# Kernel optimization log

Measured on AMD Instinct MI355X. Metric: run time of the kernel, lower is better.

Reference implementation:

```python
import jax, jax.numpy as jnp
import numpy as np

NUM_EXPERTS = 8
TOP_K = 2
N_EMBD = 1024
BLOCKING = 128
D_FFN = ((4 * N_EMBD // TOP_K) + BLOCKING - 1) // BLOCKING * BLOCKING  # 2048


def setup_inputs() -> dict:
    key = jax.random.key(0)
    k_x, k_r, k_w1, k_w2 = jax.random.split(key, 4)
    B, S = 4, 2048
    x = jax.random.normal(k_x, (B, S, N_EMBD), dtype=jnp.float32)
    # nn.Linear weight layout: [out_features, in_features]
    router_w = jax.random.normal(k_r, (NUM_EXPERTS, N_EMBD), dtype=jnp.float32) * 0.02
    # trunc_normal(std=0.02, a=-0.06, b=0.06) approximated by clipped normal
    w1 = jnp.clip(jax.random.normal(k_w1, (N_EMBD, NUM_EXPERTS * D_FFN), dtype=jnp.float32) * 0.02, -0.06, 0.06)
    w2 = jnp.clip(jax.random.normal(k_w2, (NUM_EXPERTS * D_FFN, N_EMBD), dtype=jnp.float32) * 0.02, -0.06, 0.06)
    return {"x": x, "router_w": router_w, "w1": w1, "w2": w2}


def reference(x, router_w, w1, w2):
    B, S, D = x.shape
    T = B * S
    x_flat = x.reshape(T, D)

    # Router
    router_logits = x_flat @ router_w.T                       # [T, E]
    router_probs = jax.nn.softmax(router_logits.astype(jnp.float32), axis=-1)
    expert_weights, selected_experts = jax.lax.top_k(router_probs, TOP_K)  # [T, K]
    expert_weights = expert_weights / expert_weights.sum(axis=-1, keepdims=True)
    expert_weights = expert_weights.astype(x.dtype)

    # Combine weights c[t, e] = sum_k weight[t, k] * [sel[t, k] == e]
    combine = jnp.zeros((T, NUM_EXPERTS), dtype=x.dtype)
    combine = combine.at[jnp.arange(T)[:, None], selected_experts].add(expert_weights)

    # Expert FFNs (math equivalent of block-sparse sdd/gelu/dsd + scatter-combine)
    w1r = w1.reshape(D, NUM_EXPERTS, D_FFN)
    w2r = w2.reshape(NUM_EXPERTS, D_FFN, D)
    out_flat = jnp.zeros((T, D), dtype=x.dtype)
    for e in range(NUM_EXPERTS):
        h = jax.nn.gelu(x_flat @ w1r[:, e, :], approximate=False)  # [T, d_ffn]
        out_flat = out_flat + combine[:, e:e + 1] * (h @ w2r[e])
    output = out_flat.reshape(B, S, D)

    # Aux losses
    router_z_loss = jnp.mean(jax.nn.logsumexp(router_logits, axis=-1) ** 2)
    p_i = router_probs.mean(axis=0)                           # [E]
    f_i = jnp.zeros((NUM_EXPERTS,), dtype=x.dtype).at[selected_experts.reshape(-1)].add(
        jnp.float32(1.0) / (T * TOP_K))
    load_balance_loss = NUM_EXPERTS * jnp.dot(f_i, p_i.astype(x.dtype))

    return output, router_z_loss, load_balance_loss, f_i
```

## Files before the change

### kernel.cpp

```cpp
#include <hip/hip_runtime.h>
#include <hip/hip_bf16.h>
#include <math.h>

#define T_TOK   8192
#define D_MODEL 1024
#define DFFN    2048
#define N_EXP   8
#define NASSIGN (T_TOK*2)

#define BM 128
#define BN 128
#define BK 32
#define TILE_MAX 144

#define WS_ZSUM     0
#define WS_PSUM     4
#define WS_COUNTS   64
#define WS_CURSOR   96
#define WS_OFFS     128
#define WS_NTILES   160
#define WS_TMAP     256
#define WS_SEL      4096
#define WS_WGT      69632
#define WS_AIDX     135168
#define WS_AW       200704
#define WS_XB       266240
#define WS_W1T      (WS_XB + 16777216)
#define WS_W2T      (WS_W1T + 33554432)
#define WS_H        (WS_W2T + 33554432)

typedef __attribute__((ext_vector_type(8))) short bf16x8;
typedef __attribute__((ext_vector_type(4))) float f32x4;
typedef __attribute__((ext_vector_type(4))) unsigned int u32x4;

static __device__ __forceinline__ unsigned short f2bf(float f) {
    unsigned int u = __builtin_bit_cast(unsigned int, f);
    u += 0x7fffu + ((u >> 16) & 1u);
    return (unsigned short)(u >> 16);
}

static __device__ __forceinline__ void gll16(const unsigned short* g, unsigned short* l) {
    __builtin_amdgcn_global_load_lds(
        (const __attribute__((address_space(1))) unsigned int*)g,
        (__attribute__((address_space(3))) unsigned int*)l, 16, 0, 0);
}

__global__ __launch_bounds__(256) void cvt_x_kernel(const float* __restrict__ in,
                                                    unsigned short* __restrict__ out)
{
    int i = (blockIdx.x * 256 + threadIdx.x) * 8;
    float4 a = *(const float4*)(in + i);
    float4 b = *(const float4*)(in + i + 4);
    unsigned short t[8];
    t[0]=f2bf(a.x); t[1]=f2bf(a.y); t[2]=f2bf(a.z); t[3]=f2bf(a.w);
    t[4]=f2bf(b.x); t[5]=f2bf(b.y); t[6]=f2bf(b.z); t[7]=f2bf(b.w);
    *(u32x4*)(out + i) = *(u32x4*)t;
}

__global__ __launch_bounds__(256) void transpose_cvt_kernel(
    const float* __restrict__ in, unsigned short* __restrict__ out, int K, int N)
{
    int e = blockIdx.z;
    const float* inp = in + (size_t)e * K * N;
    unsigned short* outp = out + (size_t)e * K * N;
    __shared__ unsigned short tile[64][68];
    int k0 = blockIdx.y * 64, n0 = blockIdx.x * 64;
    int tid = threadIdx.x;
    int r = tid >> 4, c4 = (tid & 15) * 4;
    #pragma unroll
    for (int p = 0; p < 4; ++p) {
        int k = r + p * 16;
        float4 v = *(const float4*)(inp + (size_t)(k0 + k) * N + n0 + c4);
        tile[k][c4+0] = f2bf(v.x);
        tile[k][c4+1] = f2bf(v.y);
        tile[k][c4+2] = f2bf(v.z);
        tile[k][c4+3] = f2bf(v.w);
    }
    __syncthreads();
    int n = tid >> 2, kc = (tid & 3) * 16;
    unsigned short t[16];
    #pragma unroll
    for (int j = 0; j < 16; ++j) t[j] = tile[kc + j][n];
    unsigned short* o = outp + (size_t)(n0 + n) * K + k0 + kc;
    *(u32x4*)o       = *(u32x4*)t;
    *(u32x4*)(o + 8) = *(u32x4*)(t + 8);
}

__global__ __launch_bounds__(256) void router_kernel(
    const float* __restrict__ x, const float* __restrict__ rw,
    float* zsum, float* psum, int* counts, int* sel, float* wgt)
{
    __shared__ float xs[32*129];
    __shared__ float rs[8*129];
    __shared__ float lg[32*9];
    __shared__ float blk_p[8];
    __shared__ int   blk_c[8];
    __shared__ float blk_z;
    int tid = threadIdx.x;
    if (tid < 8) { blk_p[tid] = 0.f; blk_c[tid] = 0; }
    if (tid == 8) blk_z = 0.f;
    int tb = blockIdx.x * 32;
    int tt = tid >> 3, e = tid & 7;
    float acc = 0.f;
    for (int c = 0; c < 8; ++c) {
        int c0 = c * 128;
        #pragma unroll
        for (int p = 0; p < 16; ++p) {
            int flat = p * 256 + tid;
            int r = flat >> 7, col = flat & 127;
            xs[r*129 + col] = x[(size_t)(tb + r)*D_MODEL + c0 + col];
        }
        #pragma unroll
        for (int p = 0; p < 4; ++p) {
            int flat = p * 256 + tid;
            int er = flat >> 7, col = flat & 127;
            rs[er*129 + col] = rw[(size_t)er*D_MODEL + c0 + col];
        }
        __syncthreads();
        #pragma unroll 8
        for (int i = 0; i < 128; ++i)
            acc += xs[tt*129 + i] * rs[e*129 + i];
        __syncthreads();
    }
    lg[tt*9 + e] = acc;
    __syncthreads();
    if (tid < 32) {
        int t = tb + tid;
        float l[8], p[8];
        float mx = -1e30f;
        #pragma unroll
        for (int j = 0; j < 8; ++j) { l[j] = lg[tid*9 + j]; mx = fmaxf(mx, l[j]); }
        float se = 0.f;
        #pragma unroll
        for (int j = 0; j < 8; ++j) { p[j] = expf(l[j] - mx); se += p[j]; }
        float inv = 1.f / se;
        #pragma unroll
        for (int j = 0; j < 8; ++j) p[j] *= inv;
        float lse = mx + logf(se);
        atomicAdd(&blk_z, lse*lse);
        #pragma unroll
        for (int j = 0; j < 8; ++j) atomicAdd(&blk_p[j], p[j]);
        int i0 = 0; float b0 = p[0];
        #pragma unroll
        for (int j = 1; j < 8; ++j) if (p[j] > b0) { b0 = p[j]; i0 = j; }
        int i1 = -1; float b1 = -1.f;
        #pragma unroll
        for (int j = 0; j < 8; ++j) if (j != i0 && p[j] > b1) { b1 = p[j]; i1 = j; }
        float s = b0 + b1;
        sel[t*2+0] = i0; sel[t*2+1] = i1;
        wgt[t*2+0] = b0 / s; wgt[t*2+1] = b1 / s;
        atomicAdd(&blk_c[i0], 1); atomicAdd(&blk_c[i1], 1);
    }
    __syncthreads();
    if (tid < 8) {
        atomicAdd(&counts[tid], blk_c[tid]);
        unsafeAtomicAdd(&psum[tid], blk_p[tid]);
    }
    if (tid == 8) unsafeAtomicAdd(zsum, blk_z);
}

__global__ void finalize_kernel(const int* counts, const float* psum, const float* zsum,
                                int* offs, int* ntiles, int* tmap, float* out_tail)
{
    if (threadIdx.x != 0) return;
    int off = 0, nt = 0;
    float lb = 0.f;
    for (int e = 0; e < N_EXP; ++e) {
        int c = counts[e];
        offs[e] = off;
        for (int m0 = 0; m0 < c; m0 += BM) {
            tmap[nt*4+0] = e;
            tmap[nt*4+1] = off + m0;
            tmap[nt*4+2] = min(BM, c - m0);
            tmap[nt*4+3] = 0;
            nt++;
        }
        float fi = (float)c / (float)NASSIGN;
        out_tail[2 + e] = fi;
        lb += fi * (psum[e] / (float)T_TOK);
        off += c;
    }
    *ntiles = nt;
    out_tail[0] = zsum[0] / (float)T_TOK;
    out_tail[1] = (float)N_EXP * lb;
}

__global__ __launch_bounds__(256) void scatter_kernel(
    const int* __restrict__ sel, const float* __restrict__ wgt,
    const int* __restrict__ offs, int* cursor, int* aidx, float* aw)
{
    int t = blockIdx.x * 256 + threadIdx.x;
    if (t >= T_TOK) return;
    #pragma unroll
    for (int k = 0; k < 2; ++k) {
        int e = sel[t*2 + k];
        int pos = atomicAdd(&cursor[e], 1);
        int r = offs[e] + pos;
        aidx[r] = t;
        aw[r] = wgt[t*2 + k];
    }
}

__global__ __launch_bounds__(256) void gemm1_kernel(
    const unsigned short* __restrict__ xb, const unsigned short* __restrict__ w1t,
    const int* __restrict__ aidx, const int* __restrict__ tmap,
    const int* __restrict__ ntiles, unsigned short* __restrict__ H)
{
    int tile = blockIdx.y;
    if (tile >= *ntiles) return;
    int e     = tmap[tile*4+0];
    int gr    = tmap[tile*4+1];
    int valid = tmap[tile*4+2];
    int n0 = blockIdx.x * BN;
    __shared__ unsigned short As[BM*BK];
    __shared__ unsigned short Bs[BN*BK];
    int tid = threadIdx.x;
    int lane = tid & 63, wave = tid >> 6;
    int wm = (wave & 1) * 64, wn = (wave >> 1) * 64;
    int q = lane >> 4, r16 = lane & 15;
    f32x4 acc[4][4];
    #pragma unroll
    for (int i = 0; i < 4; ++i)
        #pragma unroll
        for (int j = 0; j < 4; ++j) acc[i][j] = (f32x4){0.f, 0.f, 0.f, 0.f};

    int c0 = tid, c1 = 256 + tid;
    int m0c = c0 >> 2, k0c = (c0 & 3) * 8;
    int m1c = c1 >> 2, k1c = (c1 & 3) * 8;
    int tok0 = aidx[gr + min(m0c, valid - 1)];
    int tok1 = aidx[gr + min(m1c, valid - 1)];
    const unsigned short* ga0 = xb + (size_t)tok0 * D_MODEL + k0c;
    const unsigned short* ga1 = xb + (size_t)tok1 * D_MODEL + k1c;
    const unsigned short* gb0 = w1t + ((size_t)(e * DFFN + n0 + m0c)) * D_MODEL + k0c;
    const unsigned short* gb1 = w1t + ((size_t)(e * DFFN + n0 + m1c)) * D_MODEL + k1c;
    unsigned short* lA0 = As + c0 * 8;
    unsigned short* lA1 = As + c1 * 8;
    unsigned short* lB0 = Bs + c0 * 8;
    unsigned short* lB1 = Bs + c1 * 8;

    for (int kt = 0; kt < D_MODEL / BK; ++kt) {
        int kofs = kt * BK;
        gll16(ga0 + kofs, lA0);
        gll16(ga1 + kofs, lA1);
        gll16(gb0 + kofs, lB0);
        gll16(gb1 + kofs, lB1);
        __syncthreads();
        bf16x8 af[4], bfr[4];
        #pragma unroll
        for (int im = 0; im < 4; ++im)
            af[im] = *(const bf16x8*)&As[(wm + im*16 + r16)*BK + q*8];
        #pragma unroll
        for (int in = 0; in < 4; ++in)
            bfr[in] = *(const bf16x8*)&Bs[(wn + in*16 + r16)*BK + q*8];
        #pragma unroll
        for (int im = 0; im < 4; ++im)
            #pragma unroll
            for (int in = 0; in < 4; ++in)
                acc[im][in] = __builtin_amdgcn_mfma_f32_16x16x32_bf16(af[im], bfr[in], acc[im][in], 0, 0, 0);
        __syncthreads();
    }
    #pragma unroll
    for (int im = 0; im < 4; ++im) {
        #pragma unroll
        for (int reg = 0; reg < 4; ++reg) {
            int m = wm + im*16 + q*4 + reg;
            if (m < valid) {
                size_t rowbase = (size_t)(gr + m) * DFFN + n0 + wn;
                #pragma unroll
                for (int in = 0; in < 4; ++in) {
                    float v = acc[im][in][reg];
                    float g = 0.5f * v * (1.0f + erff(v * 0.70710678118654752f));
                    H[rowbase + in*16 + r16] = f2bf(g);
                }
            }
        }
    }
}

__global__ __launch_bounds__(256) void gemm2_kernel(
    const unsigned short* __restrict__ H, const unsigned short* __restrict__ w2t,
    const int* __restrict__ aidx, const float* __restrict__ aw,
    const int* __restrict__ tmap, const int* __restrict__ ntiles,
    float* __restrict__ out)
{
    int tile = blockIdx.y;
    if (tile >= *ntiles) return;
    int e     = tmap[tile*4+0];
    int gr    = tmap[tile*4+1];
    int valid = tmap[tile*4+2];
    int n0 = blockIdx.x * BN;
    __shared__ unsigned short As[BM*BK];
    __shared__ unsigned short Bs[BN*BK];
    int tid = threadIdx.x;
    int lane = tid & 63, wave = tid >> 6;
    int wm = (wave & 1) * 64, wn = (wave >> 1) * 64;
    int q = lane >> 4, r16 = lane & 15;
    f32x4 acc[4][4];
    #pragma unroll
    for (int i = 0; i < 4; ++i)
        #pragma unroll
        for (int j = 0; j < 4; ++j) acc[i][j] = (f32x4){0.f, 0.f, 0.f, 0.f};

    int c0 = tid, c1 = 256 + tid;
    int m0c = c0 >> 2, k0c = (c0 & 3) * 8;
    int m1c = c1 >> 2, k1c = (c1 & 3) * 8;
    const unsigned short* ga0 = H + (size_t)(gr + min(m0c, valid - 1)) * DFFN + k0c;
    const unsigned short* ga1 = H + (size_t)(gr + min(m1c, valid - 1)) * DFFN + k1c;
    const unsigned short* gb0 = w2t + (size_t)e * (DFFN * D_MODEL) + (size_t)(n0 + m0c) * DFFN + k0c;
    const unsigned short* gb1 = w2t + (size_t)e * (DFFN * D_MODEL) + (size_t)(n0 + m1c) * DFFN + k1c;
    unsigned short* lA0 = As + c0 * 8;
    unsigned short* lA1 = As + c1 * 8;
    unsigned short* lB0 = Bs + c0 * 8;
    unsigned short* lB1 = Bs + c1 * 8;

    for (int kt = 0; kt < DFFN / BK; ++kt) {
        int kofs = kt * BK;
        gll16(ga0 + kofs, lA0);
        gll16(ga1 + kofs, lA1);
        gll16(gb0 + kofs, lB0);
        gll16(gb1 + kofs, lB1);
        __syncthreads();
        bf16x8 af[4], bfr[4];
        #pragma unroll
        for (int im = 0; im < 4; ++im)
            af[im] = *(const bf16x8*)&As[(wm + im*16 + r16)*BK + q*8];
        #pragma unroll
        for (int in = 0; in < 4; ++in)
            bfr[in] = *(const bf16x8*)&Bs[(wn + in*16 + r16)*BK + q*8];
        #pragma unroll
        for (int im = 0; im < 4; ++im)
            #pragma unroll
            for (int in = 0; in < 4; ++in)
                acc[im][in] = __builtin_amdgcn_mfma_f32_16x16x32_bf16(af[im], bfr[in], acc[im][in], 0, 0, 0);
        __syncthreads();
    }
    #pragma unroll
    for (int im = 0; im < 4; ++im) {
        #pragma unroll
        for (int reg = 0; reg < 4; ++reg) {
            int m = wm + im*16 + q*4 + reg;
            if (m < valid) {
                int t = aidx[gr + m];
                float w = aw[gr + m];
                float* orow = out + (size_t)t*D_MODEL + n0 + wn;
                #pragma unroll
                for (int in = 0; in < 4; ++in)
                    unsafeAtomicAdd(&orow[in*16 + r16], w * acc[im][in][reg]);
            }
        }
    }
}

extern "C" void kernel_launch(void* const* d_in, const int* in_sizes, int n_in,
                              void* d_out, int out_size, void* d_ws, size_t ws_size,
                              hipStream_t stream)
{
    const float* x  = (const float*)d_in[0];
    const float* rw = (const float*)d_in[1];
    const float* w1 = (const float*)d_in[2];
    const float* w2 = (const float*)d_in[3];
    float* out = (float*)d_out;
    char* ws = (char*)d_ws;
    float* zsum   = (float*)(ws + WS_ZSUM);
    float* psum   = (float*)(ws + WS_PSUM);
    int*   counts = (int*)(ws + WS_COUNTS);
    int*   cursor = (int*)(ws + WS_CURSOR);
    int*   offs   = (int*)(ws + WS_OFFS);
    int*   ntiles = (int*)(ws + WS_NTILES);
    int*   tmap   = (int*)(ws + WS_TMAP);
    int*   sel    = (int*)(ws + WS_SEL);
    float* wgt    = (float*)(ws + WS_WGT);
    int*   aidx   = (int*)(ws + WS_AIDX);
    float* aw     = (float*)(ws + WS_AW);
    unsigned short* xb  = (unsigned short*)(ws + WS_XB);
    unsigned short* w1t = (unsigned short*)(ws + WS_W1T);
    unsigned short* w2t = (unsigned short*)(ws + WS_W2T);
    unsigned short* H   = (unsigned short*)(ws + WS_H);

    hipMemsetAsync(d_out, 0, (size_t)T_TOK * D_MODEL * sizeof(float), stream);
    hipMemsetAsync(ws, 0, 256, stream);

    cvt_x_kernel<<<T_TOK*D_MODEL/(256*8), 256, 0, stream>>>(x, xb);
    transpose_cvt_kernel<<<dim3(16384/64, 1024/64, 1), 256, 0, stream>>>(w1, w1t, 1024, 16384);
    transpose_cvt_kernel<<<dim3(1024/64, 2048/64, 8), 256, 0, stream>>>(w2, w2t, 2048, 1024);

    router_kernel<<<T_TOK/32, 256, 0, stream>>>(x, rw, zsum, psum, counts, sel, wgt);
    finalize_kernel<<<1, 64, 0, stream>>>(counts, psum, zsum, offs, ntiles, tmap,
                                          out + (size_t)T_TOK * D_MODEL);
    scatter_kernel<<<T_TOK/256, 256, 0, stream>>>(sel, wgt, offs, cursor, aidx, aw);
    gemm1_kernel<<<dim3(DFFN/BN, TILE_MAX), 256, 0, stream>>>(xb, w1t, aidx, tmap, ntiles, H);
    gemm2_kernel<<<dim3(D_MODEL/BN, TILE_MAX), 256, 0, stream>>>(H, w2t, aidx, aw, tmap, ntiles, out);
}
```

Measured before the change: 613.2 us.

## Double GEMM K-tile, swizzle LDS layout, fuse x bf16 conversion into router

Raises the GEMM K-tile from 32 to 64 so each barrier pair covers twice as many MFMAs, and stores A/B tiles in LDS with an XOR swizzle of 16-byte chunks to avoid bank conflicts on fragment reads. The standalone fp32-to-bf16 conversion kernel for x is removed; the router kernel now writes bf16 x from the shared-memory tile it already loads, saving one launch and one full read of x. LDS use per block doubles, which may reduce occupancy.

```diff
diff --git a/kernel.cpp b/kernel.cpp
--- a/kernel.cpp
+++ b/kernel.cpp
@@ -10,7 +10,7 @@
 
 #define BM 128
 #define BN 128
-#define BK 32
+#define BK 64
 #define TILE_MAX 144
 
 #define WS_ZSUM     0
@@ -45,16 +45,8 @@
         (__attribute__((address_space(3))) unsigned int*)l, 16, 0, 0);
 }
 
-__global__ __launch_bounds__(256) void cvt_x_kernel(const float* __restrict__ in,
-                                                    unsigned short* __restrict__ out)
-{
-    int i = (blockIdx.x * 256 + threadIdx.x) * 8;
-    float4 a = *(const float4*)(in + i);
-    float4 b = *(const float4*)(in + i + 4);
-    unsigned short t[8];
-    t[0]=f2bf(a.x); t[1]=f2bf(a.y); t[2]=f2bf(a.z); t[3]=f2bf(a.w);
-    t[4]=f2bf(b.x); t[5]=f2bf(b.y); t[6]=f2bf(b.z); t[7]=f2bf(b.w);
-    *(u32x4*)(out + i) = *(u32x4*)t;
+static __device__ __forceinline__ int frag_off(int row, int kc) {
+    return (row * 8 + (kc ^ (row & 7))) * 8;
 }
 
 __global__ __launch_bounds__(256) void transpose_cvt_kernel(
@@ -88,7 +80,8 @@
 
 __global__ __launch_bounds__(256) void router_kernel(
     const float* __restrict__ x, const float* __restrict__ rw,
-    float* zsum, float* psum, int* counts, int* sel, float* wgt)
+    float* zsum, float* psum, int* counts, int* sel, float* wgt,
+    unsigned short* __restrict__ xb)
 {
     __shared__ float xs[32*129];
     __shared__ float rs[8*129];
@@ -117,6 +110,15 @@
             rs[er*129 + col] = rw[(size_t)er*D_MODEL + c0 + col];
         }
         __syncthreads();
+        {
+            int rr = tid >> 3, cc = (tid & 7) * 16;
+            unsigned short tmp[16];
+            #pragma unroll
+            for (int j = 0; j < 16; ++j) tmp[j] = f2bf(xs[rr*129 + cc + j]);
+            unsigned short* o = xb + (size_t)(tb + rr)*D_MODEL + c0 + cc;
+            *(u32x4*)o       = *(u32x4*)tmp;
+            *(u32x4*)(o + 8) = *(u32x4*)(tmp + 8);
+        }
         #pragma unroll 8
         for (int i = 0; i < 128; ++i)
             acc += xs[tt*129 + i] * rs[e*129 + i];
@@ -224,39 +226,44 @@
         #pragma unroll
         for (int j = 0; j < 4; ++j) acc[i][j] = (f32x4){0.f, 0.f, 0.f, 0.f};
 
-    int c0 = tid, c1 = 256 + tid;
-    int m0c = c0 >> 2, k0c = (c0 & 3) * 8;
-    int m1c = c1 >> 2, k1c = (c1 & 3) * 8;
-    int tok0 = aidx[gr + min(m0c, valid - 1)];
-    int tok1 = aidx[gr + min(m1c, valid - 1)];
-    const unsigned short* ga0 = xb + (size_t)tok0 * D_MODEL + k0c;
-    const unsigned short* ga1 = xb + (size_t)tok1 * D_MODEL + k1c;
-    const unsigned short* gb0 = w1t + ((size_t)(e * DFFN + n0 + m0c)) * D_MODEL + k0c;
-    const unsigned short* gb1 = w1t + ((size_t)(e * DFFN + n0 + m1c)) * D_MODEL + k1c;
-    unsigned short* lA0 = As + c0 * 8;
-    unsigned short* lA1 = As + c1 * 8;
-    unsigned short* lB0 = Bs + c0 * 8;
-    unsigned short* lB1 = Bs + c1 * 8;
+    const unsigned short* aga[4];
+    const unsigned short* bga[4];
+    unsigned short* ldsA[4];
+    unsigned short* ldsB[4];
+    #pragma unroll
+    for (int j = 0; j < 4; ++j) {
+        int c = tid + j*256;
+        int m = c >> 3, kl = c & 7;
+        int kg = kl ^ (m & 7);
+        int tok = aidx[gr + min(m, valid - 1)];
+        aga[j] = xb + (size_t)tok * D_MODEL + kg*8;
+        bga[j] = w1t + ((size_t)(e * DFFN + n0 + m)) * D_MODEL + kg*8;
+        ldsA[j] = As + c*8;
+        ldsB[j] = Bs + c*8;
+    }
 
     for (int kt = 0; kt < D_MODEL / BK; ++kt) {
-        int kofs = kt * BK;
-        gll16(ga0 + kofs, lA0);
-        gll16(ga1 + kofs, lA1);
-        gll16(gb0 + kofs, lB0);
-        gll16(gb1 + kofs, lB1);
-        __syncthreads();
-        bf16x8 af[4], bfr[4];
-        #pragma unroll
-        for (int im = 0; im < 4; ++im)
-            af[im] = *(const bf16x8*)&As[(wm + im*16 + r16)*BK + q*8];
-        #pragma unroll
-        for (int in = 0; in < 4; ++in)
-            bfr[in] = *(const bf16x8*)&Bs[(wn + in*16 + r16)*BK + q*8];
-        #pragma unroll
-        for (int im = 0; im < 4; ++im)
+        int ko = kt * BK;
+        #pragma unroll
+        for (int j = 0; j < 4; ++j) gll16(aga[j] + ko, ldsA[j]);
+        #pragma unroll
+        for (int j = 0; j < 4; ++j) gll16(bga[j] + ko, ldsB[j]);
+        __syncthreads();
+        #pragma unroll
+        for (int kh = 0; kh < 2; ++kh) {
+            bf16x8 af[4], bfr[4];
+            #pragma unroll
+            for (int im = 0; im < 4; ++im)
+                af[im] = *(const bf16x8*)&As[frag_off(wm + im*16 + r16, q + 4*kh)];
             #pragma unroll
             for (int in = 0; in < 4; ++in)
-                acc[im][in] = __builtin_amdgcn_mfma_f32_16x16x32_bf16(af[im], bfr[in], acc[im][in], 0, 0, 0);
+                bfr[in] = *(const bf16x8*)&Bs[frag_off(wn + in*16 + r16, q + 4*kh)];
+            #pragma unroll
+            for (int im = 0; im < 4; ++im)
+                #pragma unroll
+                for (int in = 0; in < 4; ++in)
+                    acc[im][in] = __builtin_amdgcn_mfma_f32_16x16x32_bf16(af[im], bfr[in], acc[im][in], 0, 0, 0);
+        }
         __syncthreads();
     }
     #pragma unroll
@@ -301,37 +308,43 @@
         #pragma unroll
         for (int j = 0; j < 4; ++j) acc[i][j] = (f32x4){0.f, 0.f, 0.f, 0.f};
 
-    int c0 = tid, c1 = 256 + tid;
-    int m0c = c0 >> 2, k0c = (c0 & 3) * 8;
-    int m1c = c1 >> 2, k1c = (c1 & 3) * 8;
-    const unsigned short* ga0 = H + (size_t)(gr + min(m0c, valid - 1)) * DFFN + k0c;
-    const unsigned short* ga1 = H + (size_t)(gr + min(m1c, valid - 1)) * DFFN + k1c;
-    const unsigned short* gb0 = w2t + (size_t)e * (DFFN * D_MODEL) + (size_t)(n0 + m0c) * DFFN + k0c;
-    const unsigned short* gb1 = w2t + (size_t)e * (DFFN * D_MODEL) + (size_t)(n0 + m1c) * DFFN + k1c;
-    unsigned short* lA0 = As + c0 * 8;
-    unsigned short* lA1 = As + c1 * 8;
-    unsigned short* lB0 = Bs + c0 * 8;
-    unsigned short* lB1 = Bs + c1 * 8;
+    const unsigned short* aga[4];
+    const unsigned short* bga[4];
+    unsigned short* ldsA[4];
+    unsigned short* ldsB[4];
+    #pragma unroll
+    for (int j = 0; j < 4; ++j) {
+        int c = tid + j*256;
+        int m = c >> 3, kl = c & 7;
+        int kg = kl ^ (m & 7);
+        aga[j] = H + (size_t)(gr + min(m, valid - 1)) * DFFN + kg*8;
+        bga[j] = w2t + (size_t)e * (DFFN * D_MODEL) + (size_t)(n0 + m) * DFFN + kg*8;
+        ldsA[j] = As + c*8;
+        ldsB[j] = Bs + c*8;
+    }
 
     for (int kt = 0; kt < DFFN / BK; ++kt) {
-        int kofs = kt * BK;
-        gll16(ga0 + kofs, lA0);
-        gll16(ga1 + kofs, lA1);
-        gll16(gb0 + kofs, lB0);
-        gll16(gb1 + kofs, lB1);
-        __syncthreads();
-        bf16x8 af[4], bfr[4];
-        #pragma unroll
-        for (int im = 0; im < 4; ++im)
-            af[im] = *(const bf16x8*)&As[(wm + im*16 + r16)*BK + q*8];
-        #pragma unroll
-        for (int in = 0; in < 4; ++in)
-            bfr[in] = *(const bf16x8*)&Bs[(wn + in*16 + r16)*BK + q*8];
-        #pragma unroll
-        for (int im = 0; im < 4; ++im)
+        int ko = kt * BK;
+        #pragma unroll
+        for (int j = 0; j < 4; ++j) gll16(aga[j] + ko, ldsA[j]);
+        #pragma unroll
+        for (int j = 0; j < 4; ++j) gll16(bga[j] + ko, ldsB[j]);
+        __syncthreads();
+        #pragma unroll
+        for (int kh = 0; kh < 2; ++kh) {
+            bf16x8 af[4], bfr[4];
+            #pragma unroll
+            for (int im = 0; im < 4; ++im)
+                af[im] = *(const bf16x8*)&As[frag_off(wm + im*16 + r16, q + 4*kh)];
             #pragma unroll
             for (int in = 0; in < 4; ++in)
-                acc[im][in] = __builtin_amdgcn_mfma_f32_16x16x32_bf16(af[im], bfr[in], acc[im][in], 0, 0, 0);
+                bfr[in] = *(const bf16x8*)&Bs[frag_off(wn + in*16 + r16, q + 4*kh)];
+            #pragma unroll
+            for (int im = 0; im < 4; ++im)
+                #pragma unroll
+                for (int in = 0; in < 4; ++in)
+                    acc[im][in] = __builtin_amdgcn_mfma_f32_16x16x32_bf16(af[im], bfr[in], acc[im][in], 0, 0, 0);
+        }
         __syncthreads();
     }
     #pragma unroll
@@ -380,11 +393,10 @@
     hipMemsetAsync(d_out, 0, (size_t)T_TOK * D_MODEL * sizeof(float), stream);
     hipMemsetAsync(ws, 0, 256, stream);
 
-    cvt_x_kernel<<<T_TOK*D_MODEL/(256*8), 256, 0, stream>>>(x, xb);
     transpose_cvt_kernel<<<dim3(16384/64, 1024/64, 1), 256, 0, stream>>>(w1, w1t, 1024, 16384);
     transpose_cvt_kernel<<<dim3(1024/64, 2048/64, 8), 256, 0, stream>>>(w2, w2t, 2048, 1024);
 
-    router_kernel<<<T_TOK/32, 256, 0, stream>>>(x, rw, zsum, psum, counts, sel, wgt);
+    router_kernel<<<T_TOK/32, 256, 0, stream>>>(x, rw, zsum, psum, counts, sel, wgt, xb);
     finalize_kernel<<<1, 64, 0, stream>>>(counts, psum, zsum, offs, ntiles, tmap,
                                           out + (size_t)T_TOK * D_MODEL);
     scatter_kernel<<<T_TOK/256, 256, 0, stream>>>(sel, wgt, offs, cursor, aidx, aw);
```

New measurement: 597.2 us. 2.6% less time.
